# Optimization experiments

Hardware: AMD Instinct MI355X
Metric: run time of the kernel (lower is better)

## Reference

```python
import jax, jax.numpy as jnp
import numpy as np

N = 8192
IN_F = 256
HID = 256
ALPHA = 0.2  # LeakyReLU negative slope


def setup_inputs() -> dict:
    key = jax.random.key(0)
    k1, k2, k3, k4 = jax.random.split(key, 4)
    src = jax.random.normal(k1, (N, IN_F), dtype=jnp.float32)
    bias = jax.random.normal(k2, (N, N), dtype=jnp.float32)
    # xavier_uniform-like init (gain 1.414)
    limW = 1.414 * np.sqrt(6.0 / (IN_F + HID))
    W = jax.random.uniform(k3, (IN_F, HID), minval=-limW, maxval=limW, dtype=jnp.float32)
    lima = 1.414 * np.sqrt(6.0 / (2 * HID + 1))
    a = jax.random.uniform(k4, (2 * HID, 1), minval=-lima, maxval=lima, dtype=jnp.float32)
    return {"src": src, "bias": bias, "W": W, "a": a}


def reference(src, bias, W, a):
    # h: [N, HID]
    h = src @ W
    # The original concatenates [h_i || h_j] and multiplies by a (2H x 1).
    # Equivalent: e_ij = h_i @ a1 + h_j @ a2, computed via two [N] vectors
    # broadcast to [N, N] — no O(N^2 * 2H) concat materialized.
    a1 = a[:HID, 0]   # [HID]
    a2 = a[HID:, 0]   # [HID]
    e = (h @ a1)[:, None] + (h @ a2)[None, :]          # [N, N]
    e = jnp.where(e > 0, e, ALPHA * e)                  # LeakyReLU
    e = e + bias
    attention = jax.nn.softmax(e, axis=-1)              # [N, N]
    return attention
```

## Files before the change

kernel.cpp:

```cpp
#include <hip/hip_runtime.h>
#include <math.h>

#define N 8192
#define IN_F 256
#define HID 256
#define ALPHA 0.2f

__global__ void compute_wa(const float* __restrict__ W, const float* __restrict__ a,
                           float* __restrict__ wa ) {
    const int m = blockIdx.x;
    const int lane = threadIdx.x;
    const float4 w  = ((const float4*)(W + m * HID))[lane];
    const float4 a1 = ((const float4*)(a))[lane];
    const float4 a2 = ((const float4*)(a + HID))[lane];
    float s1 = w.x * a1.x + w.y * a1.y + w.z * a1.z + w.w * a1.w;
    float s2 = w.x * a2.x + w.y * a2.y + w.z * a2.z + w.w * a2.w;
#pragma unroll
    for (int off = 32; off > 0; off >>= 1) {
        s1 += __shfl_xor(s1, off);
        s2 += __shfl_xor(s2, off);
    }
    if (lane == 0) {
        wa[m]       = s1;
        wa[HID + m] = s2;
    }
}

__global__ void compute_f(const float* __restrict__ src, const float* __restrict__ wa,
                          float* __restrict__ f1, float* __restrict__ f2) {
    const int wave = threadIdx.x >> 6;
    const int lane = threadIdx.x & 63;
    const int row  = blockIdx.x * 4 + wave;
    const float4 v  = ((const float4*)(src + (size_t)row * IN_F))[lane];
    const float4 x1 = ((const float4*)(wa))[lane];
    const float4 x2 = ((const float4*)(wa + HID))[lane];
    float s1 = v.x * x1.x + v.y * x1.y + v.z * x1.z + v.w * x1.w;
    float s2 = v.x * x2.x + v.y * x2.y + v.z * x2.z + v.w * x2.w;
#pragma unroll
    for (int off = 32; off > 0; off >>= 1) {
        s1 += __shfl_xor(s1, off);
        s2 += __shfl_xor(s2, off);
    }
    if (lane == 0) {
        f1[row] = s1;
        f2[row] = s2;
    }
}

__global__ __launch_bounds__(256) void attn_softmax(
    const float* __restrict__ bias, const float* __restrict__ f1,
    const float* __restrict__ f2, float* __restrict__ out) {
    const int row = blockIdx.x;
    const int t   = threadIdx.x;
    const float f1i = f1[row];

    const float4* __restrict__ brow = (const float4*)(bias + (size_t)row * N);
    const float4* __restrict__ f2v  = (const float4*)f2;
    float4* __restrict__ orow       = (float4*)(out + (size_t)row * N);

    float e[32];
    float lmax = -3.4e38f;
#pragma unroll
    for (int u = 0; u < 8; ++u) {
        const int idx = u * 256 + t;
        const float4 b = brow[idx];
        const float4 g = f2v[idx];
        float4 v;
        v.x = f1i + g.x; v.y = f1i + g.y; v.z = f1i + g.z; v.w = f1i + g.w;
        v.x = (v.x > 0.f ? v.x : ALPHA * v.x) + b.x;
        v.y = (v.y > 0.f ? v.y : ALPHA * v.y) + b.y;
        v.z = (v.z > 0.f ? v.z : ALPHA * v.z) + b.z;
        v.w = (v.w > 0.f ? v.w : ALPHA * v.w) + b.w;
        e[u * 4 + 0] = v.x; e[u * 4 + 1] = v.y;
        e[u * 4 + 2] = v.z; e[u * 4 + 3] = v.w;
        lmax = fmaxf(lmax, fmaxf(fmaxf(v.x, v.y), fmaxf(v.z, v.w)));
    }

    __shared__ float smax[4];
    __shared__ float ssum[4];
    const int wave = t >> 6, lane = t & 63;

#pragma unroll
    for (int off = 32; off > 0; off >>= 1) lmax = fmaxf(lmax, __shfl_xor(lmax, off));
    if (lane == 0) smax[wave] = lmax;
    __syncthreads();
    const float gmax = fmaxf(fmaxf(smax[0], smax[1]), fmaxf(smax[2], smax[3]));

    float lsum = 0.f;
#pragma unroll
    for (int i = 0; i < 32; ++i) {
        e[i] = __expf(e[i] - gmax);
        lsum += e[i];
    }
#pragma unroll
    for (int off = 32; off > 0; off >>= 1) lsum += __shfl_xor(lsum, off);
    if (lane == 0) ssum[wave] = lsum;
    __syncthreads();
    const float inv = 1.f / (ssum[0] + ssum[1] + ssum[2] + ssum[3]);

#pragma unroll
    for (int u = 0; u < 8; ++u) {
        const int idx = u * 256 + t;
        float4 v;
        v.x = e[u * 4 + 0] * inv; v.y = e[u * 4 + 1] * inv;
        v.z = e[u * 4 + 2] * inv; v.w = e[u * 4 + 3] * inv;
        orow[idx] = v;
    }
}

extern "C" void kernel_launch(void* const* d_in, const int* in_sizes, int n_in,
                              void* d_out, int out_size, void* d_ws, size_t ws_size,
                              hipStream_t stream) {
    const float* src  = (const float*)d_in[0];
    const float* bias = (const float*)d_in[1];
    const float* W    = (const float*)d_in[2];
    const float* a    = (const float*)d_in[3];
    float* out = (float*)d_out;

    float* ws = (float*)d_ws;
    float* wa = ws;
    float* f1 = ws + 512;
    float* f2 = ws + 512 + N;

    compute_wa<<<HID, 64, 0, stream>>>(W, a, wa);
    compute_f<<<N / 4, 256, 0, stream>>>(src, wa, f1, f2);
    attn_softmax<<<N, 256, 0, stream>>>(bias, f1, f2, out);
}
```

Measured before the change: 108.1 us.

## Use 512-thread rows, single-barrier online softmax, nontemporal bias/output access

```diff
diff --git a/kernel.cpp b/kernel.cpp
--- a/kernel.cpp
+++ b/kernel.cpp
@@ -5,6 +5,8 @@
 #define IN_F 256
 #define HID 256
 #define ALPHA 0.2f
+
+typedef float f32x4 __attribute__((ext_vector_type(4)));
 
 __global__ void compute_wa(const float* __restrict__ W, const float* __restrict__ a,
                            float* __restrict__ wa ) {
@@ -47,26 +49,25 @@
     }
 }
 
-__global__ __launch_bounds__(256) void attn_softmax(
+__global__ __launch_bounds__(512) void attn_softmax(
     const float* __restrict__ bias, const float* __restrict__ f1,
     const float* __restrict__ f2, float* __restrict__ out) {
     const int row = blockIdx.x;
     const int t   = threadIdx.x;
     const float f1i = f1[row];
 
-    const float4* __restrict__ brow = (const float4*)(bias + (size_t)row * N);
-    const float4* __restrict__ f2v  = (const float4*)f2;
-    float4* __restrict__ orow       = (float4*)(out + (size_t)row * N);
+    const f32x4* __restrict__ brow = (const f32x4*)(bias + (size_t)row * N);
+    const f32x4* __restrict__ f2v  = (const f32x4*)f2;
+    f32x4* __restrict__ orow       = (f32x4*)(out + (size_t)row * N);
 
-    float e[32];
+    float e[16];
     float lmax = -3.4e38f;
 #pragma unroll
-    for (int u = 0; u < 8; ++u) {
-        const int idx = u * 256 + t;
-        const float4 b = brow[idx];
-        const float4 g = f2v[idx];
-        float4 v;
-        v.x = f1i + g.x; v.y = f1i + g.y; v.z = f1i + g.z; v.w = f1i + g.w;
+    for (int u = 0; u < 4; ++u) {
+        const int idx = u * 512 + t;
+        const f32x4 b = __builtin_nontemporal_load(&brow[idx]);
+        const f32x4 g = f2v[idx];
+        f32x4 v = f1i + g;
         v.x = (v.x > 0.f ? v.x : ALPHA * v.x) + b.x;
         v.y = (v.y > 0.f ? v.y : ALPHA * v.y) + b.y;
         v.z = (v.z > 0.f ? v.z : ALPHA * v.z) + b.z;
@@ -76,35 +77,39 @@
         lmax = fmaxf(lmax, fmaxf(fmaxf(v.x, v.y), fmaxf(v.z, v.w)));
     }
 
-    __shared__ float smax[4];
-    __shared__ float ssum[4];
-    const int wave = t >> 6, lane = t & 63;
-
 #pragma unroll
     for (int off = 32; off > 0; off >>= 1) lmax = fmaxf(lmax, __shfl_xor(lmax, off));
-    if (lane == 0) smax[wave] = lmax;
-    __syncthreads();
-    const float gmax = fmaxf(fmaxf(smax[0], smax[1]), fmaxf(smax[2], smax[3]));
 
     float lsum = 0.f;
 #pragma unroll
-    for (int i = 0; i < 32; ++i) {
-        e[i] = __expf(e[i] - gmax);
+    for (int i = 0; i < 16; ++i) {
+        e[i] = __expf(e[i] - lmax);
         lsum += e[i];
     }
 #pragma unroll
     for (int off = 32; off > 0; off >>= 1) lsum += __shfl_xor(lsum, off);
-    if (lane == 0) ssum[wave] = lsum;
+
+    __shared__ float wm[8];
+    __shared__ float wsum[8];
+    const int wave = t >> 6, lane = t & 63;
+    if (lane == 0) { wm[wave] = lmax; wsum[wave] = lsum; }
     __syncthreads();
-    const float inv = 1.f / (ssum[0] + ssum[1] + ssum[2] + ssum[3]);
+
+    float M = wm[0];
+#pragma unroll
+    for (int w = 1; w < 8; ++w) M = fmaxf(M, wm[w]);
+    float S = 0.f;
+#pragma unroll
+    for (int w = 0; w < 8; ++w) S += wsum[w] * __expf(wm[w] - M);
+    const float scale = __expf(lmax - M) / S;
 
 #pragma unroll
-    for (int u = 0; u < 8; ++u) {
-        const int idx = u * 256 + t;
-        float4 v;
-        v.x = e[u * 4 + 0] * inv; v.y = e[u * 4 + 1] * inv;
-        v.z = e[u * 4 + 2] * inv; v.w = e[u * 4 + 3] * inv;
-        orow[idx] = v;
+    for (int u = 0; u < 4; ++u) {
+        const int idx = u * 512 + t;
+        f32x4 v;
+        v.x = e[u * 4 + 0] * scale; v.y = e[u * 4 + 1] * scale;
+        v.z = e[u * 4 + 2] * scale; v.w = e[u * 4 + 3] * scale;
+        __builtin_nontemporal_store(v, &orow[idx]);
     }
 }
 
@@ -124,5 +129,5 @@
 
     compute_wa<<<HID, 64, 0, stream>>>(W, a, wa);
     compute_f<<<N / 4, 256, 0, stream>>>(src, wa, f1, f2);
-    attn_softmax<<<N, 256, 0, stream>>>(bias, f1, f2, out);
+    attn_softmax<<<N, 512, 0, stream>>>(bias, f1, f2, out);
 }
```

Measured after the change: 99.69 us. -7.8%, faster.
